# Performance work log

Measured on AMD Instinct MI355X. Metric: run time of the kernel, lower is better.

## Reference

```python
import jax, jax.numpy as jnp
import numpy as np

B, T, H = 2048, 512, 16  # batch, seq_len, lstm hidden


def _lstm_step(h, c, x_t, W_ih, W_hh, b):
    # PyTorch gate order: i, f, g, o ; z: [B, 4H]
    z = x_t @ W_ih.T + h @ W_hh.T + b
    i, f, g, o = jnp.split(z, 4, axis=-1)
    c = jax.nn.sigmoid(f) * c + jax.nn.sigmoid(i) * jnp.tanh(g)
    h = jax.nn.sigmoid(o) * jnp.tanh(c)
    return h, c


def setup_inputs() -> dict:
    key = jax.random.key(0)
    ks = jax.random.split(key, 14)
    s = 1.0 / np.sqrt(H)  # torch default uniform init bound
    u = lambda k, shp: jax.random.uniform(k, shp, jnp.float32, -s, s)
    return {
        "x": jax.random.normal(ks[0], (B, T, 1), jnp.float32),
        # forward-direction LSTM params
        "W_ih_f": u(ks[1], (4 * H, 1)),
        "W_hh_f": u(ks[2], (4 * H, H)),
        "b_ih_f": u(ks[3], (4 * H,)),
        "b_hh_f": u(ks[4], (4 * H,)),
        # reverse-direction LSTM params
        "W_ih_r": u(ks[5], (4 * H, 1)),
        "W_hh_r": u(ks[6], (4 * H, H)),
        "b_ih_r": u(ks[7], (4 * H,)),
        "b_hh_r": u(ks[8], (4 * H,)),
        # MLP head (Dropout is identity at inference)
        "W1": u(ks[9], (16, 32)),
        "b1": u(ks[10], (16,)),
        "W2": u(ks[11], (1, 16)),
        "b2": u(ks[12], (1,)),
    }


def reference(x, W_ih_f, W_hh_f, b_ih_f, b_hh_f,
              W_ih_r, W_hh_r, b_ih_r, b_hh_r, W1, b1, W2, b2):
    Bv = x.shape[0]
    h0 = jnp.zeros((Bv, H), x.dtype)
    b_f = b_ih_f + b_hh_f

    # forward direction: out[:, -1, :H] is the final forward hidden state
    def step(carry, x_t):
        h, c = carry
        h, c = _lstm_step(h, c, x_t, W_ih_f, W_hh_f, b_f)
        return (h, c), None

    (h_fwd, _), _ = jax.lax.scan(step, (h0, h0), jnp.swapaxes(x, 0, 1))

    # reverse direction at t = T-1 is the FIRST step of the reverse scan,
    # i.e. one LSTM step on x[:, -1] from zero state (only part sliced by out[:, -1]).
    h_bwd, _ = _lstm_step(h0, h0, x[:, -1], W_ih_r, W_hh_r, b_ih_r + b_hh_r)

    h_cat = jnp.concatenate([h_fwd, h_bwd], axis=-1)  # [B, 32]
    # Dropout(0.5) is identity in eval mode
    hid = h_cat @ W1.T + b1
    hid = jnp.where(hid > 0, hid, 0.2 * hid)  # LeakyReLU(0.2)
    return hid @ W2.T + b2  # [B, 1]
```

## Files before the change

### kernel.cpp

```cpp
#include <hip/hip_runtime.h>

#define T_LEN 512
#define LOG2E 1.4426950408889634f

typedef float f32x2 __attribute__((ext_vector_type(2)));

__device__ __forceinline__ float rl(float v, int lane) {
    return __int_as_float(__builtin_amdgcn_readlane(__float_as_int(v), lane));
}
template<int CTRL>
__device__ __forceinline__ float qperm(float v) {
    return __int_as_float(__builtin_amdgcn_mov_dpp(__float_as_int(v), CTRL, 0xF, 0xF, true));
}

__global__ __launch_bounds__(256, 2) void bilstm_head_kernel(
    const float* __restrict__ x,
    const float* __restrict__ W_ih_f, const float* __restrict__ W_hh_f,
    const float* __restrict__ b_ih_f, const float* __restrict__ b_hh_f,
    const float* __restrict__ W_ih_r, const float* __restrict__ W_hh_r,
    const float* __restrict__ b_ih_r, const float* __restrict__ b_hh_r,
    const float* __restrict__ W1, const float* __restrict__ b1,
    const float* __restrict__ W2, const float* __restrict__ b2,
    float* __restrict__ out)
{
    extern __shared__ float smem[];

    const int tid  = threadIdx.x;
    const int wid  = tid >> 6;
    const int lane = tid & 63;
    const int b    = blockIdx.x * 4 + wid;

    const int gate = lane & 3;
    const int k    = lane >> 2;
    const int row  = gate * 16 + k;

    const bool  isg = (gate == 2);
    const float c1  = isg ? (-2.0f * LOG2E) : (-LOG2E);
    const float cm  = isg ? 2.0f : 1.0f;
    const float ca  = isg ? -1.0f : 0.0f;
    const float k2  = -2.0f * LOG2E;

    const float wih_p  = W_ih_f[row] * c1;
    const float bias_p = (b_ih_f[row] + b_hh_f[row]) * c1;
    f32x2 wp[8];
#pragma unroll
    for (int n = 0; n < 8; ++n) {
        wp[n].x = W_hh_f[row * 16 + 2 * n]     * c1;
        wp[n].y = W_hh_f[row * 16 + 2 * n + 1] * c1;
    }

    const int wfl = wid * 592;
#pragma unroll
    for (int i = 0; i < 8; ++i)
        smem[wfl + 64 + i * 64 + lane] = x[b * T_LEN + i * 64 + lane];

    const unsigned hbase = (unsigned)(wfl * 4);
    unsigned xaddr = hbase + 224;
    const unsigned waddr = hbase + (unsigned)(row * 4);
    float c = 0.0f;

#define LSTM_STEP(XC, XN, XOFF) \
    "s_waitcnt lgkmcnt(5)\n\t" \
    "v_fma_f32 v20, " XC ", %[wih], %[bias]\n\t" \
    "v_mov_b32 v21, 0\n\t" \
    "s_waitcnt lgkmcnt(3)\n\t" \
    "v_pk_fma_f32 v[20:21], v[32:33], %[w01], v[20:21]\n\t" \
    "v_pk_fma_f32 v[20:21], v[34:35], %[w23], v[20:21]\n\t" \
    "s_waitcnt lgkmcnt(2)\n\t" \
    "v_pk_fma_f32 v[20:21], v[36:37], %[w45], v[20:21]\n\t" \
    "v_pk_fma_f32 v[20:21], v[38:39], %[w67], v[20:21]\n\t" \
    "s_waitcnt lgkmcnt(1)\n\t" \
    "v_pk_mul_f32 v[24:25], v[40:41], %[w89]\n\t" \
    "v_pk_fma_f32 v[24:25], v[42:43], %[wAB], v[24:25]\n\t" \
    "s_waitcnt lgkmcnt(0)\n\t" \
    "v_pk_fma_f32 v[24:25], v[44:45], %[wCD], v[24:25]\n\t" \
    "v_pk_fma_f32 v[24:25], v[46:47], %[wEF], v[24:25]\n\t" \
    "v_add_f32 v20, v20, v24\n\t" \
    "v_add_f32 v21, v21, v25\n\t" \
    "v_add_f32 v20, v20, v21\n\t" \
    "v_exp_f32 v22, v20\n\t" \
    "ds_read_b32 " XN ", %[vX] offset:" XOFF "\n\t" \
    "s_nop 0\n\t" \
    "v_add_f32 v22, 1.0, v22\n\t" \
    "v_rcp_f32 v22, v22\n\t" \
    "s_nop 1\n\t" \
    "v_fma_f32 v23, v22, %[cm], %[ca]\n\t" \
    "s_nop 1\n\t" \
    "v_mov_b32_dpp v26, v23 quad_perm:[1,0,3,2] row_mask:0xf bank_mask:0xf\n\t" \
    "v_mov_b32_dpp v27, v23 quad_perm:[2,3,0,1] row_mask:0xf bank_mask:0xf\n\t" \
    "v_mov_b32_dpp v28, v23 quad_perm:[3,2,1,0] row_mask:0xf bank_mask:0xf\n\t" \
    "v_mul_f32 v22, v23, v27\n\t" \
    "v_fma_f32 %[c], v26, %[c], v22\n\t" \
    "v_mul_f32 v22, %[k2], %[c]\n\t" \
    "v_exp_f32 v22, v22\n\t" \
    "s_nop 1\n\t" \
    "v_add_f32 v22, 1.0, v22\n\t" \
    "v_rcp_f32 v22, v22\n\t" \
    "s_nop 1\n\t" \
    "v_fma_f32 v22, v22, 2.0, -1.0\n\t" \
    "v_mul_f32 v29, v28, v22\n\t" \
    "ds_write_b32 %[vW], v29\n\t" \
    "ds_read_b128 v[32:35], %[vB] offset:0\n\t" \
    "ds_read_b128 v[36:39], %[vB] offset:16\n\t" \
    "ds_read_b128 v[40:43], %[vB] offset:32\n\t" \
    "ds_read_b128 v[44:47], %[vB] offset:48\n\t"

    asm volatile(
        "v_mov_b32 v29, 0\n\t"
        "ds_read_b32 v30, %[vB] offset:256\n\t"
        "ds_write_b32 %[vW], v29\n\t"
        "ds_read_b128 v[32:35], %[vB] offset:0\n\t"
        "ds_read_b128 v[36:39], %[vB] offset:16\n\t"
        "ds_read_b128 v[40:43], %[vB] offset:32\n\t"
        "ds_read_b128 v[44:47], %[vB] offset:48\n\t"
        "s_mov_b32 s20, 0\n\t"
        "1:\n\t"
        "v_add_u32 %[vX], 32, %[vX]\n\t"
        LSTM_STEP("v30", "v31", "4")
        LSTM_STEP("v31", "v30", "8")
        LSTM_STEP("v30", "v31", "12")
        LSTM_STEP("v31", "v30", "16")
        LSTM_STEP("v30", "v31", "20")
        LSTM_STEP("v31", "v30", "24")
        LSTM_STEP("v30", "v31", "28")
        LSTM_STEP("v31", "v30", "32")
        "s_add_u32 s20, s20, 1\n\t"
        "s_cmp_lt_u32 s20, 64\n\t"
        "s_cbranch_scc1 1b\n\t"
        "s_waitcnt lgkmcnt(0)\n\t"
        : [c]"+v"(c), [vX]"+v"(xaddr)
        : [vB]"v"(hbase), [vW]"v"(waddr),
          [wih]"v"(wih_p), [bias]"v"(bias_p),
          [cm]"v"(cm), [ca]"v"(ca), [k2]"v"(k2),
          [w01]"v"(wp[0]), [w23]"v"(wp[1]), [w45]"v"(wp[2]), [w67]"v"(wp[3]),
          [w89]"v"(wp[4]), [wAB]"v"(wp[5]), [wCD]"v"(wp[6]), [wEF]"v"(wp[7])
        : "v20","v21","v22","v23","v24","v25","v26","v27","v28","v29",
          "v30","v31","v32","v33","v34","v35","v36","v37","v38","v39",
          "v40","v41","v42","v43","v44","v45","v46","v47",
          "s20","scc","memory");
#undef LSTM_STEP

    float hs[16];
#pragma unroll
    for (int n = 0; n < 16; ++n) hs[n] = smem[wfl + n];

    const float wihr  = W_ih_r[row];
    const float biasr = b_ih_r[row] + b_hh_r[row];
    const float xlast = smem[wfl + 64 + 511];

    const float zr   = fmaf(xlast, wihr, biasr);
    const float er   = __builtin_amdgcn_exp2f(zr * c1);
    const float rr_  = __builtin_amdgcn_rcpf(1.0f + er);
    const float actr = fmaf(rr_, cm, ca);
    const float gr   = qperm<0x4E>(actr);
    const float or_  = qperm<0x1B>(actr);
    const float cr   = actr * gr;
    const float e2r  = __builtin_amdgcn_exp2f(cr * (-2.0f * LOG2E));
    const float thr_ = fmaf(__builtin_amdgcn_rcpf(1.0f + e2r), 2.0f, -1.0f);
    const float hbw  = or_ * thr_;

    float hr[16];
#pragma unroll
    for (int n = 0; n < 16; ++n) hr[n] = rl(hbw, 4 * n);

    const int m = lane & 15;
    float hid = b1[m];
#pragma unroll
    for (int n = 0; n < 16; ++n) hid = fmaf(hs[n], W1[m * 32 + n], hid);
#pragma unroll
    for (int n = 0; n < 16; ++n) hid = fmaf(hr[n], W1[m * 32 + 16 + n], hid);
    hid = (hid > 0.0f) ? hid : (0.2f * hid);

    float v = hid * W2[m];
    v += __shfl_xor(v, 1);
    v += __shfl_xor(v, 2);
    v += __shfl_xor(v, 4);
    v += __shfl_xor(v, 8);
    if (lane == 0) out[b] = v + b2[0];
}

extern "C" void kernel_launch(void* const* d_in, const int* in_sizes, int n_in,
                              void* d_out, int out_size, void* d_ws, size_t ws_size,
                              hipStream_t stream) {
    const float* x      = (const float*)d_in[0];
    const float* W_ih_f = (const float*)d_in[1];
    const float* W_hh_f = (const float*)d_in[2];
    const float* b_ih_f = (const float*)d_in[3];
    const float* b_hh_f = (const float*)d_in[4];
    const float* W_ih_r = (const float*)d_in[5];
    const float* W_hh_r = (const float*)d_in[6];
    const float* b_ih_r = (const float*)d_in[7];
    const float* b_hh_r = (const float*)d_in[8];
    const float* W1     = (const float*)d_in[9];
    const float* b1     = (const float*)d_in[10];
    const float* W2     = (const float*)d_in[11];
    const float* b2     = (const float*)d_in[12];
    float* out = (float*)d_out;

    const int B = in_sizes[0] / T_LEN;
    dim3 grid(B / 4), block(256);
    size_t lds_bytes = 4 * 592 * sizeof(float);
    hipLaunchKernelGGL(bilstm_head_kernel, grid, block, lds_bytes, stream,
                       x, W_ih_f, W_hh_f, b_ih_f, b_hh_f,
                       W_ih_r, W_hh_r, b_ih_r, b_hh_r,
                       W1, b1, W2, b2, out);
}
```

Baseline: 82.38 us.

## Pack two batch rows per wavefront with two gate rows per lane

```diff
diff --git a/kernel.cpp b/kernel.cpp
--- a/kernel.cpp
+++ b/kernel.cpp
@@ -5,15 +5,7 @@
 
 typedef float f32x2 __attribute__((ext_vector_type(2)));
 
-__device__ __forceinline__ float rl(float v, int lane) {
-    return __int_as_float(__builtin_amdgcn_readlane(__float_as_int(v), lane));
-}
-template<int CTRL>
-__device__ __forceinline__ float qperm(float v) {
-    return __int_as_float(__builtin_amdgcn_mov_dpp(__float_as_int(v), CTRL, 0xF, 0xF, true));
-}
-
-__global__ __launch_bounds__(256, 2) void bilstm_head_kernel(
+__global__ __launch_bounds__(256, 1) void bilstm_head_kernel(
     const float* __restrict__ x,
     const float* __restrict__ W_ih_f, const float* __restrict__ W_hh_f,
     const float* __restrict__ b_ih_f, const float* __restrict__ b_hh_f,
@@ -28,77 +20,94 @@
     const int tid  = threadIdx.x;
     const int wid  = tid >> 6;
     const int lane = tid & 63;
-    const int b    = blockIdx.x * 4 + wid;
-
-    const int gate = lane & 3;
-    const int k    = lane >> 2;
-    const int row  = gate * 16 + k;
-
-    const bool  isg = (gate == 2);
-    const float c1  = isg ? (-2.0f * LOG2E) : (-LOG2E);
-    const float cm  = isg ? 2.0f : 1.0f;
-    const float ca  = isg ? -1.0f : 0.0f;
-    const float k2  = -2.0f * LOG2E;
-
-    const float wih_p  = W_ih_f[row] * c1;
-    const float bias_p = (b_ih_f[row] + b_hh_f[row]) * c1;
-    f32x2 wp[8];
+    const int half = lane >> 5;
+    const int hl   = lane & 31;
+    const int b    = blockIdx.x * 8 + wid * 2 + half;
+
+    const int k = hl >> 1;
+    const int p = hl & 1;
+    const int row0 = p * 16 + k;
+    const int row1 = (2 + p) * 16 + k;
+
+    const float c1_0 = -LOG2E;
+    const float c1_1 = (p == 0) ? (-2.0f * LOG2E) : (-LOG2E);
+    const float cm1  = (p == 0) ? 2.0f : 1.0f;
+    const float ca1  = (p == 0) ? -1.0f : 0.0f;
+    const float k2   = -2.0f * LOG2E;
+
+    const float wih0  = W_ih_f[row0] * c1_0;
+    const float bias0 = (b_ih_f[row0] + b_hh_f[row0]) * c1_0;
+    const float wih1  = W_ih_f[row1] * c1_1;
+    const float bias1 = (b_ih_f[row1] + b_hh_f[row1]) * c1_1;
+    f32x2 w0p[8], w1p[8];
 #pragma unroll
     for (int n = 0; n < 8; ++n) {
-        wp[n].x = W_hh_f[row * 16 + 2 * n]     * c1;
-        wp[n].y = W_hh_f[row * 16 + 2 * n + 1] * c1;
+        w0p[n].x = W_hh_f[row0 * 16 + 2 * n]     * c1_0;
+        w0p[n].y = W_hh_f[row0 * 16 + 2 * n + 1] * c1_0;
+        w1p[n].x = W_hh_f[row1 * 16 + 2 * n]     * c1_1;
+        w1p[n].y = W_hh_f[row1 * 16 + 2 * n + 1] * c1_1;
     }
 
-    const int wfl = wid * 592;
-#pragma unroll
-    for (int i = 0; i < 8; ++i)
-        smem[wfl + 64 + i * 64 + lane] = x[b * T_LEN + i * 64 + lane];
-
-    const unsigned hbase = (unsigned)(wfl * 4);
-    unsigned xaddr = hbase + 224;
-    const unsigned waddr = hbase + (unsigned)(row * 4);
+    const int rbase = (wid * 2 + half) * 560;
+#pragma unroll
+    for (int i = 0; i < 16; ++i)
+        smem[rbase + 32 + i * 32 + hl] = x[b * T_LEN + i * 32 + hl];
+
+    const unsigned vB = (unsigned)(rbase * 4);
+    const unsigned vW = (unsigned)((rbase + p * 16 + k) * 4);
+    unsigned vX = (unsigned)(rbase * 4 + 96);
     float c = 0.0f;
 
 #define LSTM_STEP(XC, XN, XOFF) \
     "s_waitcnt lgkmcnt(5)\n\t" \
-    "v_fma_f32 v20, " XC ", %[wih], %[bias]\n\t" \
+    "v_fma_f32 v20, " XC ", %[wih0], %[bias0]\n\t" \
     "v_mov_b32 v21, 0\n\t" \
+    "v_fma_f32 v22, " XC ", %[wih1], %[bias1]\n\t" \
+    "v_mov_b32 v23, 0\n\t" \
     "s_waitcnt lgkmcnt(3)\n\t" \
-    "v_pk_fma_f32 v[20:21], v[32:33], %[w01], v[20:21]\n\t" \
-    "v_pk_fma_f32 v[20:21], v[34:35], %[w23], v[20:21]\n\t" \
+    "v_pk_fma_f32 v[20:21], v[32:33], %[w00], v[20:21]\n\t" \
+    "v_pk_fma_f32 v[22:23], v[32:33], %[w10], v[22:23]\n\t" \
+    "v_pk_fma_f32 v[20:21], v[34:35], %[w01], v[20:21]\n\t" \
+    "v_pk_fma_f32 v[22:23], v[34:35], %[w11], v[22:23]\n\t" \
     "s_waitcnt lgkmcnt(2)\n\t" \
-    "v_pk_fma_f32 v[20:21], v[36:37], %[w45], v[20:21]\n\t" \
-    "v_pk_fma_f32 v[20:21], v[38:39], %[w67], v[20:21]\n\t" \
+    "v_pk_fma_f32 v[20:21], v[36:37], %[w02], v[20:21]\n\t" \
+    "v_pk_fma_f32 v[22:23], v[36:37], %[w12], v[22:23]\n\t" \
+    "v_pk_fma_f32 v[20:21], v[38:39], %[w03], v[20:21]\n\t" \
+    "v_pk_fma_f32 v[22:23], v[38:39], %[w13], v[22:23]\n\t" \
     "s_waitcnt lgkmcnt(1)\n\t" \
-    "v_pk_mul_f32 v[24:25], v[40:41], %[w89]\n\t" \
-    "v_pk_fma_f32 v[24:25], v[42:43], %[wAB], v[24:25]\n\t" \
+    "v_pk_fma_f32 v[20:21], v[40:41], %[w04], v[20:21]\n\t" \
+    "v_pk_fma_f32 v[22:23], v[40:41], %[w14], v[22:23]\n\t" \
+    "v_pk_fma_f32 v[20:21], v[42:43], %[w05], v[20:21]\n\t" \
+    "v_pk_fma_f32 v[22:23], v[42:43], %[w15], v[22:23]\n\t" \
     "s_waitcnt lgkmcnt(0)\n\t" \
-    "v_pk_fma_f32 v[24:25], v[44:45], %[wCD], v[24:25]\n\t" \
-    "v_pk_fma_f32 v[24:25], v[46:47], %[wEF], v[24:25]\n\t" \
-    "v_add_f32 v20, v20, v24\n\t" \
-    "v_add_f32 v21, v21, v25\n\t" \
+    "v_pk_fma_f32 v[20:21], v[44:45], %[w06], v[20:21]\n\t" \
+    "v_pk_fma_f32 v[22:23], v[44:45], %[w16], v[22:23]\n\t" \
+    "v_pk_fma_f32 v[20:21], v[46:47], %[w07], v[20:21]\n\t" \
+    "v_pk_fma_f32 v[22:23], v[46:47], %[w17], v[22:23]\n\t" \
     "v_add_f32 v20, v20, v21\n\t" \
-    "v_exp_f32 v22, v20\n\t" \
+    "v_add_f32 v22, v22, v23\n\t" \
+    "v_exp_f32 v24, v20\n\t" \
+    "v_exp_f32 v25, v22\n\t" \
     "ds_read_b32 " XN ", %[vX] offset:" XOFF "\n\t" \
-    "s_nop 0\n\t" \
-    "v_add_f32 v22, 1.0, v22\n\t" \
-    "v_rcp_f32 v22, v22\n\t" \
-    "s_nop 1\n\t" \
-    "v_fma_f32 v23, v22, %[cm], %[ca]\n\t" \
-    "s_nop 1\n\t" \
-    "v_mov_b32_dpp v26, v23 quad_perm:[1,0,3,2] row_mask:0xf bank_mask:0xf\n\t" \
-    "v_mov_b32_dpp v27, v23 quad_perm:[2,3,0,1] row_mask:0xf bank_mask:0xf\n\t" \
-    "v_mov_b32_dpp v28, v23 quad_perm:[3,2,1,0] row_mask:0xf bank_mask:0xf\n\t" \
-    "v_mul_f32 v22, v23, v27\n\t" \
-    "v_fma_f32 %[c], v26, %[c], v22\n\t" \
-    "v_mul_f32 v22, %[k2], %[c]\n\t" \
-    "v_exp_f32 v22, v22\n\t" \
-    "s_nop 1\n\t" \
-    "v_add_f32 v22, 1.0, v22\n\t" \
-    "v_rcp_f32 v22, v22\n\t" \
-    "s_nop 1\n\t" \
-    "v_fma_f32 v22, v22, 2.0, -1.0\n\t" \
-    "v_mul_f32 v29, v28, v22\n\t" \
+    "v_add_f32 v24, 1.0, v24\n\t" \
+    "v_add_f32 v25, 1.0, v25\n\t" \
+    "v_rcp_f32 v24, v24\n\t" \
+    "v_rcp_f32 v25, v25\n\t" \
+    "s_nop 1\n\t" \
+    "v_fma_f32 v25, v25, %[cm1], %[ca1]\n\t" \
+    "s_nop 1\n\t" \
+    "v_mov_b32_dpp v26, v24 quad_perm:[1,0,3,2] row_mask:0xf bank_mask:0xf\n\t" \
+    "v_mov_b32_dpp v27, v25 quad_perm:[1,0,3,2] row_mask:0xf bank_mask:0xf\n\t" \
+    "v_mul_f32 v28, v24, v25\n\t" \
+    "v_fma_f32 %[c], v26, %[c], v28\n\t" \
+    "v_mul_f32 v28, %[k2], %[c]\n\t" \
+    "v_exp_f32 v28, v28\n\t" \
+    "s_nop 1\n\t" \
+    "v_add_f32 v28, 1.0, v28\n\t" \
+    "v_rcp_f32 v28, v28\n\t" \
+    "s_nop 1\n\t" \
+    "v_fma_f32 v28, v28, 2.0, -1.0\n\t" \
+    "v_mul_f32 v29, v27, v28\n\t" \
     "ds_write_b32 %[vW], v29\n\t" \
     "ds_read_b128 v[32:35], %[vB] offset:0\n\t" \
     "ds_read_b128 v[36:39], %[vB] offset:16\n\t" \
@@ -107,7 +116,7 @@
 
     asm volatile(
         "v_mov_b32 v29, 0\n\t"
-        "ds_read_b32 v30, %[vB] offset:256\n\t"
+        "ds_read_b32 v30, %[vB] offset:128\n\t"
         "ds_write_b32 %[vW], v29\n\t"
         "ds_read_b128 v[32:35], %[vB] offset:0\n\t"
         "ds_read_b128 v[36:39], %[vB] offset:16\n\t"
@@ -128,47 +137,42 @@
         "s_cmp_lt_u32 s20, 64\n\t"
         "s_cbranch_scc1 1b\n\t"
         "s_waitcnt lgkmcnt(0)\n\t"
-        : [c]"+v"(c), [vX]"+v"(xaddr)
-        : [vB]"v"(hbase), [vW]"v"(waddr),
-          [wih]"v"(wih_p), [bias]"v"(bias_p),
-          [cm]"v"(cm), [ca]"v"(ca), [k2]"v"(k2),
-          [w01]"v"(wp[0]), [w23]"v"(wp[1]), [w45]"v"(wp[2]), [w67]"v"(wp[3]),
-          [w89]"v"(wp[4]), [wAB]"v"(wp[5]), [wCD]"v"(wp[6]), [wEF]"v"(wp[7])
+        : [c]"+v"(c), [vX]"+v"(vX)
+        : [vB]"v"(vB), [vW]"v"(vW),
+          [wih0]"v"(wih0), [bias0]"v"(bias0),
+          [wih1]"v"(wih1), [bias1]"v"(bias1),
+          [cm1]"v"(cm1), [ca1]"v"(ca1), [k2]"v"(k2),
+          [w00]"v"(w0p[0]), [w01]"v"(w0p[1]), [w02]"v"(w0p[2]), [w03]"v"(w0p[3]),
+          [w04]"v"(w0p[4]), [w05]"v"(w0p[5]), [w06]"v"(w0p[6]), [w07]"v"(w0p[7]),
+          [w10]"v"(w1p[0]), [w11]"v"(w1p[1]), [w12]"v"(w1p[2]), [w13]"v"(w1p[3]),
+          [w14]"v"(w1p[4]), [w15]"v"(w1p[5]), [w16]"v"(w1p[6]), [w17]"v"(w1p[7])
         : "v20","v21","v22","v23","v24","v25","v26","v27","v28","v29",
           "v30","v31","v32","v33","v34","v35","v36","v37","v38","v39",
           "v40","v41","v42","v43","v44","v45","v46","v47",
           "s20","scc","memory");
 #undef LSTM_STEP
 
-    float hs[16];
-#pragma unroll
-    for (int n = 0; n < 16; ++n) hs[n] = smem[wfl + n];
-
-    const float wihr  = W_ih_r[row];
-    const float biasr = b_ih_r[row] + b_hh_r[row];
-    const float xlast = smem[wfl + 64 + 511];
-
-    const float zr   = fmaf(xlast, wihr, biasr);
-    const float er   = __builtin_amdgcn_exp2f(zr * c1);
-    const float rr_  = __builtin_amdgcn_rcpf(1.0f + er);
-    const float actr = fmaf(rr_, cm, ca);
-    const float gr   = qperm<0x4E>(actr);
-    const float or_  = qperm<0x1B>(actr);
-    const float cr   = actr * gr;
-    const float e2r  = __builtin_amdgcn_exp2f(cr * (-2.0f * LOG2E));
-    const float thr_ = fmaf(__builtin_amdgcn_rcpf(1.0f + e2r), 2.0f, -1.0f);
-    const float hbw  = or_ * thr_;
-
-    float hr[16];
-#pragma unroll
-    for (int n = 0; n < 16; ++n) hr[n] = rl(hbw, 4 * n);
-
-    const int m = lane & 15;
+    if (hl < 16) {
+        const int j = hl;
+        const float xl = smem[rbase + 32 + 511];
+        const float zi = fmaf(xl, W_ih_r[j],      b_ih_r[j]      + b_hh_r[j]);
+        const float zg = fmaf(xl, W_ih_r[32 + j], b_ih_r[32 + j] + b_hh_r[32 + j]);
+        const float zo = fmaf(xl, W_ih_r[48 + j], b_ih_r[48 + j] + b_hh_r[48 + j]);
+        const float si = __builtin_amdgcn_rcpf(1.0f + __builtin_amdgcn_exp2f(-zi * LOG2E));
+        const float tg = fmaf(__builtin_amdgcn_rcpf(1.0f + __builtin_amdgcn_exp2f(-2.0f * zg * LOG2E)), 2.0f, -1.0f);
+        const float so = __builtin_amdgcn_rcpf(1.0f + __builtin_amdgcn_exp2f(-zo * LOG2E));
+        const float cr = si * tg;
+        const float th = fmaf(__builtin_amdgcn_rcpf(1.0f + __builtin_amdgcn_exp2f(-2.0f * cr * LOG2E)), 2.0f, -1.0f);
+        smem[rbase + 16 + j] = so * th;
+    }
+    __syncthreads();
+
+    const int m = hl & 15;
     float hid = b1[m];
 #pragma unroll
-    for (int n = 0; n < 16; ++n) hid = fmaf(hs[n], W1[m * 32 + n], hid);
-#pragma unroll
-    for (int n = 0; n < 16; ++n) hid = fmaf(hr[n], W1[m * 32 + 16 + n], hid);
+    for (int n = 0; n < 16; ++n) hid = fmaf(smem[rbase + n],      W1[m * 32 + n],      hid);
+#pragma unroll
+    for (int n = 0; n < 16; ++n) hid = fmaf(smem[rbase + 16 + n], W1[m * 32 + 16 + n], hid);
     hid = (hid > 0.0f) ? hid : (0.2f * hid);
 
     float v = hid * W2[m];
@@ -176,7 +180,7 @@
     v += __shfl_xor(v, 2);
     v += __shfl_xor(v, 4);
     v += __shfl_xor(v, 8);
-    if (lane == 0) out[b] = v + b2[0];
+    if (hl == 0) out[b] = v + b2[0];
 }
 
 extern "C" void kernel_launch(void* const* d_in, const int* in_sizes, int n_in,
@@ -198,8 +202,8 @@
     float* out = (float*)d_out;
 
     const int B = in_sizes[0] / T_LEN;
-    dim3 grid(B / 4), block(256);
-    size_t lds_bytes = 4 * 592 * sizeof(float);
+    dim3 grid(B / 8), block(256);
+    size_t lds_bytes = 8 * 560 * sizeof(float);
     hipLaunchKernelGGL(bilstm_head_kernel, grid, block, lds_bytes, stream,
                        x, W_ih_f, W_hh_f, b_ih_f, b_hh_f,
                        W_ih_r, W_hh_r, b_ih_r, b_hh_r,
```

Result: faster. 72.84 us (-11.6%).

## Interleave two independent batch LSTM recurrences per wavefront to hide latency

Applied to the files above, without the earlier changes.

```diff
diff --git a/kernel.cpp b/kernel.cpp
--- a/kernel.cpp
+++ b/kernel.cpp
@@ -5,15 +5,7 @@
 
 typedef float f32x2 __attribute__((ext_vector_type(2)));
 
-__device__ __forceinline__ float rl(float v, int lane) {
-    return __int_as_float(__builtin_amdgcn_readlane(__float_as_int(v), lane));
-}
-template<int CTRL>
-__device__ __forceinline__ float qperm(float v) {
-    return __int_as_float(__builtin_amdgcn_mov_dpp(__float_as_int(v), CTRL, 0xF, 0xF, true));
-}
-
-__global__ __launch_bounds__(256, 2) void bilstm_head_kernel(
+__global__ __launch_bounds__(256, 1) void bilstm_head_kernel(
     const float* __restrict__ x,
     const float* __restrict__ W_ih_f, const float* __restrict__ W_hh_f,
     const float* __restrict__ b_ih_f, const float* __restrict__ b_hh_f,
@@ -28,7 +20,8 @@
     const int tid  = threadIdx.x;
     const int wid  = tid >> 6;
     const int lane = tid & 63;
-    const int b    = blockIdx.x * 4 + wid;
+    const int bA   = blockIdx.x * 8 + wid * 2;
+    const int bB   = bA + 1;
 
     const int gate = lane & 3;
     const int k    = lane >> 2;
@@ -49,134 +42,184 @@
         wp[n].y = W_hh_f[row * 16 + 2 * n + 1] * c1;
     }
 
-    const int wfl = wid * 592;
-#pragma unroll
-    for (int i = 0; i < 8; ++i)
-        smem[wfl + 64 + i * 64 + lane] = x[b * T_LEN + i * 64 + lane];
-
-    const unsigned hbase = (unsigned)(wfl * 4);
-    unsigned xaddr = hbase + 224;
-    const unsigned waddr = hbase + (unsigned)(row * 4);
-    float c = 0.0f;
-
-#define LSTM_STEP(XC, XN, XOFF) \
-    "s_waitcnt lgkmcnt(5)\n\t" \
+    const int rA = (wid * 2)     * 592;
+    const int rB = (wid * 2 + 1) * 592;
+#pragma unroll
+    for (int i = 0; i < 8; ++i) {
+        smem[rA + 64 + i * 64 + lane] = x[bA * T_LEN + i * 64 + lane];
+        smem[rB + 64 + i * 64 + lane] = x[bB * T_LEN + i * 64 + lane];
+    }
+
+    const unsigned vBA = (unsigned)(rA * 4);
+    const unsigned vBB = (unsigned)(rB * 4);
+    const unsigned vWA = vBA + (unsigned)(row * 4);
+    const unsigned vWB = vBB + (unsigned)(row * 4);
+    unsigned vXA = vBA + 224;
+    unsigned vXB = vBB + 224;
+    float cA = 0.0f, cB = 0.0f;
+
+#define STEP_A(XC, XN, XOFF) \
+    "s_waitcnt lgkmcnt(6)\n\t" \
     "v_fma_f32 v20, " XC ", %[wih], %[bias]\n\t" \
     "v_mov_b32 v21, 0\n\t" \
-    "s_waitcnt lgkmcnt(3)\n\t" \
+    "v_pk_mul_f32 v[22:23], v[40:41], %[w89]\n\t" \
     "v_pk_fma_f32 v[20:21], v[32:33], %[w01], v[20:21]\n\t" \
+    "v_pk_fma_f32 v[22:23], v[42:43], %[wAB], v[22:23]\n\t" \
     "v_pk_fma_f32 v[20:21], v[34:35], %[w23], v[20:21]\n\t" \
-    "s_waitcnt lgkmcnt(2)\n\t" \
+    "v_pk_fma_f32 v[22:23], v[44:45], %[wCD], v[22:23]\n\t" \
     "v_pk_fma_f32 v[20:21], v[36:37], %[w45], v[20:21]\n\t" \
+    "v_pk_fma_f32 v[22:23], v[46:47], %[wEF], v[22:23]\n\t" \
     "v_pk_fma_f32 v[20:21], v[38:39], %[w67], v[20:21]\n\t" \
-    "s_waitcnt lgkmcnt(1)\n\t" \
-    "v_pk_mul_f32 v[24:25], v[40:41], %[w89]\n\t" \
-    "v_pk_fma_f32 v[24:25], v[42:43], %[wAB], v[24:25]\n\t" \
-    "s_waitcnt lgkmcnt(0)\n\t" \
-    "v_pk_fma_f32 v[24:25], v[44:45], %[wCD], v[24:25]\n\t" \
-    "v_pk_fma_f32 v[24:25], v[46:47], %[wEF], v[24:25]\n\t" \
-    "v_add_f32 v20, v20, v24\n\t" \
-    "v_add_f32 v21, v21, v25\n\t" \
+    "v_add_f32 v20, v20, v22\n\t" \
+    "v_add_f32 v21, v21, v23\n\t" \
     "v_add_f32 v20, v20, v21\n\t" \
-    "v_exp_f32 v22, v20\n\t" \
-    "ds_read_b32 " XN ", %[vX] offset:" XOFF "\n\t" \
+    "v_exp_f32 v24, v20\n\t" \
+    "ds_read_b32 " XN ", %[vXA] offset:" XOFF "\n\t" \
     "s_nop 0\n\t" \
-    "v_add_f32 v22, 1.0, v22\n\t" \
-    "v_rcp_f32 v22, v22\n\t" \
-    "s_nop 1\n\t" \
-    "v_fma_f32 v23, v22, %[cm], %[ca]\n\t" \
-    "s_nop 1\n\t" \
-    "v_mov_b32_dpp v26, v23 quad_perm:[1,0,3,2] row_mask:0xf bank_mask:0xf\n\t" \
-    "v_mov_b32_dpp v27, v23 quad_perm:[2,3,0,1] row_mask:0xf bank_mask:0xf\n\t" \
-    "v_mov_b32_dpp v28, v23 quad_perm:[3,2,1,0] row_mask:0xf bank_mask:0xf\n\t" \
-    "v_mul_f32 v22, v23, v27\n\t" \
-    "v_fma_f32 %[c], v26, %[c], v22\n\t" \
-    "v_mul_f32 v22, %[k2], %[c]\n\t" \
-    "v_exp_f32 v22, v22\n\t" \
-    "s_nop 1\n\t" \
-    "v_add_f32 v22, 1.0, v22\n\t" \
-    "v_rcp_f32 v22, v22\n\t" \
-    "s_nop 1\n\t" \
-    "v_fma_f32 v22, v22, 2.0, -1.0\n\t" \
-    "v_mul_f32 v29, v28, v22\n\t" \
-    "ds_write_b32 %[vW], v29\n\t" \
-    "ds_read_b128 v[32:35], %[vB] offset:0\n\t" \
-    "ds_read_b128 v[36:39], %[vB] offset:16\n\t" \
-    "ds_read_b128 v[40:43], %[vB] offset:32\n\t" \
-    "ds_read_b128 v[44:47], %[vB] offset:48\n\t"
+    "v_add_f32 v24, 1.0, v24\n\t" \
+    "v_rcp_f32 v24, v24\n\t" \
+    "s_nop 1\n\t" \
+    "v_fma_f32 v25, v24, %[cm], %[ca]\n\t" \
+    "s_nop 1\n\t" \
+    "v_mov_b32_dpp v26, v25 quad_perm:[1,0,3,2] row_mask:0xf bank_mask:0xf\n\t" \
+    "v_mov_b32_dpp v27, v25 quad_perm:[2,3,0,1] row_mask:0xf bank_mask:0xf\n\t" \
+    "v_mov_b32_dpp v28, v25 quad_perm:[3,2,1,0] row_mask:0xf bank_mask:0xf\n\t" \
+    "v_mul_f32 v24, v25, v27\n\t" \
+    "v_fma_f32 %[cA], v26, %[cA], v24\n\t" \
+    "v_mul_f32 v24, %[k2], %[cA]\n\t" \
+    "v_exp_f32 v24, v24\n\t" \
+    "s_nop 1\n\t" \
+    "v_add_f32 v24, 1.0, v24\n\t" \
+    "v_rcp_f32 v24, v24\n\t" \
+    "s_nop 1\n\t" \
+    "v_fma_f32 v24, v24, 2.0, -1.0\n\t" \
+    "v_mul_f32 v29, v28, v24\n\t" \
+    "ds_write_b32 %[vWA], v29\n\t" \
+    "ds_read_b128 v[32:35], %[vBA] offset:0\n\t" \
+    "ds_read_b128 v[36:39], %[vBA] offset:16\n\t" \
+    "ds_read_b128 v[40:43], %[vBA] offset:32\n\t" \
+    "ds_read_b128 v[44:47], %[vBA] offset:48\n\t"
+
+#define STEP_B(XC, XN, XOFF) \
+    "s_waitcnt lgkmcnt(6)\n\t" \
+    "v_fma_f32 v20, " XC ", %[wih], %[bias]\n\t" \
+    "v_mov_b32 v21, 0\n\t" \
+    "v_pk_mul_f32 v[22:23], v[56:57], %[w89]\n\t" \
+    "v_pk_fma_f32 v[20:21], v[48:49], %[w01], v[20:21]\n\t" \
+    "v_pk_fma_f32 v[22:23], v[58:59], %[wAB], v[22:23]\n\t" \
+    "v_pk_fma_f32 v[20:21], v[50:51], %[w23], v[20:21]\n\t" \
+    "v_pk_fma_f32 v[22:23], v[60:61], %[wCD], v[22:23]\n\t" \
+    "v_pk_fma_f32 v[20:21], v[52:53], %[w45], v[20:21]\n\t" \
+    "v_pk_fma_f32 v[22:23], v[62:63], %[wEF], v[22:23]\n\t" \
+    "v_pk_fma_f32 v[20:21], v[54:55], %[w67], v[20:21]\n\t" \
+    "v_add_f32 v20, v20, v22\n\t" \
+    "v_add_f32 v21, v21, v23\n\t" \
+    "v_add_f32 v20, v20, v21\n\t" \
+    "v_exp_f32 v24, v20\n\t" \
+    "ds_read_b32 " XN ", %[vXB] offset:" XOFF "\n\t" \
+    "s_nop 0\n\t" \
+    "v_add_f32 v24, 1.0, v24\n\t" \
+    "v_rcp_f32 v24, v24\n\t" \
+    "s_nop 1\n\t" \
+    "v_fma_f32 v25, v24, %[cm], %[ca]\n\t" \
+    "s_nop 1\n\t" \
+    "v_mov_b32_dpp v26, v25 quad_perm:[1,0,3,2] row_mask:0xf bank_mask:0xf\n\t" \
+    "v_mov_b32_dpp v27, v25 quad_perm:[2,3,0,1] row_mask:0xf bank_mask:0xf\n\t" \
+    "v_mov_b32_dpp v28, v25 quad_perm:[3,2,1,0] row_mask:0xf bank_mask:0xf\n\t" \
+    "v_mul_f32 v24, v25, v27\n\t" \
+    "v_fma_f32 %[cB], v26, %[cB], v24\n\t" \
+    "v_mul_f32 v24, %[k2], %[cB]\n\t" \
+    "v_exp_f32 v24, v24\n\t" \
+    "s_nop 1\n\t" \
+    "v_add_f32 v24, 1.0, v24\n\t" \
+    "v_rcp_f32 v24, v24\n\t" \
+    "s_nop 1\n\t" \
+    "v_fma_f32 v24, v24, 2.0, -1.0\n\t" \
+    "v_mul_f32 v29, v28, v24\n\t" \
+    "ds_write_b32 %[vWB], v29\n\t" \
+    "ds_read_b128 v[48:51], %[vBB] offset:0\n\t" \
+    "ds_read_b128 v[52:55], %[vBB] offset:16\n\t" \
+    "ds_read_b128 v[56:59], %[vBB] offset:32\n\t" \
+    "ds_read_b128 v[60:63], %[vBB] offset:48\n\t"
 
     asm volatile(
         "v_mov_b32 v29, 0\n\t"
-        "ds_read_b32 v30, %[vB] offset:256\n\t"
-        "ds_write_b32 %[vW], v29\n\t"
-        "ds_read_b128 v[32:35], %[vB] offset:0\n\t"
-        "ds_read_b128 v[36:39], %[vB] offset:16\n\t"
-        "ds_read_b128 v[40:43], %[vB] offset:32\n\t"
-        "ds_read_b128 v[44:47], %[vB] offset:48\n\t"
+        "ds_read_b32 v30, %[vBA] offset:256\n\t"
+        "ds_write_b32 %[vWA], v29\n\t"
+        "ds_read_b128 v[32:35], %[vBA] offset:0\n\t"
+        "ds_read_b128 v[36:39], %[vBA] offset:16\n\t"
+        "ds_read_b128 v[40:43], %[vBA] offset:32\n\t"
+        "ds_read_b128 v[44:47], %[vBA] offset:48\n\t"
+        "ds_read_b32 v18, %[vBB] offset:256\n\t"
+        "ds_write_b32 %[vWB], v29\n\t"
+        "ds_read_b128 v[48:51], %[vBB] offset:0\n\t"
+        "ds_read_b128 v[52:55], %[vBB] offset:16\n\t"
+        "ds_read_b128 v[56:59], %[vBB] offset:32\n\t"
+        "ds_read_b128 v[60:63], %[vBB] offset:48\n\t"
         "s_mov_b32 s20, 0\n\t"
         "1:\n\t"
-        "v_add_u32 %[vX], 32, %[vX]\n\t"
-        LSTM_STEP("v30", "v31", "4")
-        LSTM_STEP("v31", "v30", "8")
-        LSTM_STEP("v30", "v31", "12")
-        LSTM_STEP("v31", "v30", "16")
-        LSTM_STEP("v30", "v31", "20")
-        LSTM_STEP("v31", "v30", "24")
-        LSTM_STEP("v30", "v31", "28")
-        LSTM_STEP("v31", "v30", "32")
+        "v_add_u32 %[vXA], 32, %[vXA]\n\t"
+        "v_add_u32 %[vXB], 32, %[vXB]\n\t"
+        STEP_A("v30", "v31", "4")  STEP_B("v18", "v19", "4")
+        STEP_A("v31", "v30", "8")  STEP_B("v19", "v18", "8")
+        STEP_A("v30", "v31", "12") STEP_B("v18", "v19", "12")
+        STEP_A("v31", "v30", "16") STEP_B("v19", "v18", "16")
+        STEP_A("v30", "v31", "20") STEP_B("v18", "v19", "20")
+        STEP_A("v31", "v30", "24") STEP_B("v19", "v18", "24")
+        STEP_A("v30", "v31", "28") STEP_B("v18", "v19", "28")
+        STEP_A("v31", "v30", "32") STEP_B("v19", "v18", "32")
         "s_add_u32 s20, s20, 1\n\t"
         "s_cmp_lt_u32 s20, 64\n\t"
         "s_cbranch_scc1 1b\n\t"
         "s_waitcnt lgkmcnt(0)\n\t"
-        : [c]"+v"(c), [vX]"+v"(xaddr)
-        : [vB]"v"(hbase), [vW]"v"(waddr),
+        : [cA]"+v"(cA), [cB]"+v"(cB), [vXA]"+v"(vXA), [vXB]"+v"(vXB)
+        : [vBA]"v"(vBA), [vBB]"v"(vBB), [vWA]"v"(vWA), [vWB]"v"(vWB),
           [wih]"v"(wih_p), [bias]"v"(bias_p),
           [cm]"v"(cm), [ca]"v"(ca), [k2]"v"(k2),
           [w01]"v"(wp[0]), [w23]"v"(wp[1]), [w45]"v"(wp[2]), [w67]"v"(wp[3]),
           [w89]"v"(wp[4]), [wAB]"v"(wp[5]), [wCD]"v"(wp[6]), [wEF]"v"(wp[7])
-        : "v20","v21","v22","v23","v24","v25","v26","v27","v28","v29",
+        : "v18","v19","v20","v21","v22","v23","v24","v25","v26","v27","v28","v29",
           "v30","v31","v32","v33","v34","v35","v36","v37","v38","v39",
           "v40","v41","v42","v43","v44","v45","v46","v47",
+          "v48","v49","v50","v51","v52","v53","v54","v55",
+          "v56","v57","v58","v59","v60","v61","v62","v63",
           "s20","scc","memory");
-#undef LSTM_STEP
-
-    float hs[16];
-#pragma unroll
-    for (int n = 0; n < 16; ++n) hs[n] = smem[wfl + n];
-
-    const float wihr  = W_ih_r[row];
-    const float biasr = b_ih_r[row] + b_hh_r[row];
-    const float xlast = smem[wfl + 64 + 511];
-
-    const float zr   = fmaf(xlast, wihr, biasr);
-    const float er   = __builtin_amdgcn_exp2f(zr * c1);
-    const float rr_  = __builtin_amdgcn_rcpf(1.0f + er);
-    const float actr = fmaf(rr_, cm, ca);
-    const float gr   = qperm<0x4E>(actr);
-    const float or_  = qperm<0x1B>(actr);
-    const float cr   = actr * gr;
-    const float e2r  = __builtin_amdgcn_exp2f(cr * (-2.0f * LOG2E));
-    const float thr_ = fmaf(__builtin_amdgcn_rcpf(1.0f + e2r), 2.0f, -1.0f);
-    const float hbw  = or_ * thr_;
-
-    float hr[16];
-#pragma unroll
-    for (int n = 0; n < 16; ++n) hr[n] = rl(hbw, 4 * n);
-
-    const int m = lane & 15;
-    float hid = b1[m];
-#pragma unroll
-    for (int n = 0; n < 16; ++n) hid = fmaf(hs[n], W1[m * 32 + n], hid);
-#pragma unroll
-    for (int n = 0; n < 16; ++n) hid = fmaf(hr[n], W1[m * 32 + 16 + n], hid);
+#undef STEP_A
+#undef STEP_B
+
+    if (lane < 32) {
+        const int rb = (lane < 16) ? rA : rB;
+        const int j  = lane & 15;
+        const float xl = smem[rb + 64 + 511];
+        const float zi = fmaf(xl, W_ih_r[j],      b_ih_r[j]      + b_hh_r[j]);
+        const float zg = fmaf(xl, W_ih_r[32 + j], b_ih_r[32 + j] + b_hh_r[32 + j]);
+        const float zo = fmaf(xl, W_ih_r[48 + j], b_ih_r[48 + j] + b_hh_r[48 + j]);
+        const float si = __builtin_amdgcn_rcpf(1.0f + __builtin_amdgcn_exp2f(-zi * LOG2E));
+        const float tg = fmaf(__builtin_amdgcn_rcpf(1.0f + __builtin_amdgcn_exp2f(-2.0f * zg * LOG2E)), 2.0f, -1.0f);
+        const float so = __builtin_amdgcn_rcpf(1.0f + __builtin_amdgcn_exp2f(-zo * LOG2E));
+        const float cr = si * tg;
+        const float th = fmaf(__builtin_amdgcn_rcpf(1.0f + __builtin_amdgcn_exp2f(-2.0f * cr * LOG2E)), 2.0f, -1.0f);
+        smem[rb + 16 + j] = so * th;
+    }
+    __syncthreads();
+
+    const int j  = lane & 15;
+    const int g  = (lane >> 4) & 1;
+    const int rb = g ? rB : rA;
+    const int bo = g ? bB : bA;
+    float hid = b1[j];
+#pragma unroll
+    for (int n = 0; n < 16; ++n) hid = fmaf(smem[rb + n],      W1[j * 32 + n],      hid);
+#pragma unroll
+    for (int n = 0; n < 16; ++n) hid = fmaf(smem[rb + 16 + n], W1[j * 32 + 16 + n], hid);
     hid = (hid > 0.0f) ? hid : (0.2f * hid);
 
-    float v = hid * W2[m];
+    float v = hid * W2[j];
     v += __shfl_xor(v, 1);
     v += __shfl_xor(v, 2);
     v += __shfl_xor(v, 4);
     v += __shfl_xor(v, 8);
-    if (lane == 0) out[b] = v + b2[0];
+    if (j == 0 && lane < 32) out[bo] = v + b2[0];
 }
 
 extern "C" void kernel_launch(void* const* d_in, const int* in_sizes, int n_in,
@@ -198,8 +241,8 @@
     float* out = (float*)d_out;
 
     const int B = in_sizes[0] / T_LEN;
-    dim3 grid(B / 4), block(256);
-    size_t lds_bytes = 4 * 592 * sizeof(float);
+    dim3 grid(B / 8), block(256);
+    size_t lds_bytes = 8 * 592 * sizeof(float);
     hipLaunchKernelGGL(bilstm_head_kernel, grid, block, lds_bytes, stream,
                        x, W_ih_f, W_hh_f, b_ih_f, b_hh_f,
                        W_ih_r, W_hh_r, b_ih_r, b_hh_r,
```

After: 103.7 us. 25.9% more time.
